# Performance work log

Hardware: AMD Instinct MI355X
Metric: run time of the kernel (lower is better)

## Reference

```python
import jax, jax.numpy as jnp
import numpy as np

B, T, D = 2, 2048, 1024
H = 16
DK = D // H


def setup_inputs() -> dict:
    key = jax.random.key(0)
    ks = jax.random.split(key, 5)
    s = 1.0 / np.sqrt(D)
    return {
        "x": jax.random.normal(ks[0], (B, T, D), dtype=jnp.float32),
        "Wq": jax.random.normal(ks[1], (D, D), dtype=jnp.float32) * s,
        "bq": jnp.zeros((D,), dtype=jnp.float32),
        "Wk": jax.random.normal(ks[2], (D, D), dtype=jnp.float32) * s,
        "bk": jnp.zeros((D,), dtype=jnp.float32),
        "Wv": jax.random.normal(ks[3], (D, D), dtype=jnp.float32) * s,
        "bv": jnp.zeros((D,), dtype=jnp.float32),
        "Wo": jax.random.normal(ks[4], (D, D), dtype=jnp.float32) * s,
        "bo": jnp.zeros((D,), dtype=jnp.float32),
    }


def reference(x, Wq, bq, Wk, bk, Wv, bv, Wo, bo):
    # projections (torch Linear: x @ W.T + b; here W is stored as (in, out))
    Q = x @ Wq + bq  # (B,T,D)
    K = x @ Wk + bk
    V = x @ Wv + bv
    # split heads -> (B,H,T,dk)
    Q = Q.reshape(B, T, H, DK).transpose(0, 2, 1, 3)
    K = K.reshape(B, T, H, DK).transpose(0, 2, 1, 3)
    V = V.reshape(B, T, H, DK).transpose(0, 2, 1, 3)
    scale = 1.0 / jnp.sqrt(jnp.asarray(DK, dtype=x.dtype))
    scores = jnp.einsum("bhqd,bhkd->bhqk", Q, K) * scale  # (B,H,T,T)
    causal = jnp.tril(jnp.ones((T, T), dtype=bool))
    scores = jnp.where(causal, scores, -jnp.inf)
    weights = jax.nn.softmax(scores, axis=-1)
    # dropout is identity in eval mode
    context = jnp.einsum("bhqk,bhkd->bhqd", weights, V)
    context = context.transpose(0, 2, 1, 3).reshape(B, T, D)
    return context @ Wo + bo
```

## Files before the change

kernel.cpp:

```cpp
#include <hip/hip_runtime.h>
#include <hip/hip_bf16.h>

constexpr int Bc = 2;
constexpr int Tc = 2048;
constexpr int Mc = Bc * Tc;
constexpr float CfQ = 0.18033688011112042f;

typedef __attribute__((ext_vector_type(8))) __bf16 bf16x8;
typedef __attribute__((ext_vector_type(4))) __bf16 bf16x4;
typedef __attribute__((ext_vector_type(4))) float floatx4;

__device__ __forceinline__ void gl_lds16(const void* g, void* l) {
    __builtin_amdgcn_global_load_lds(
        (const __attribute__((address_space(1))) void*)g,
        (__attribute__((address_space(3))) void*)l, 16, 0, 0);
}

__global__ __launch_bounds__(256) void prep_all(const float* __restrict__ x,
                                                const float* __restrict__ Wq,
                                                const float* __restrict__ Wk,
                                                const float* __restrict__ Wv,
                                                const float* __restrict__ Wo,
                                                __bf16* __restrict__ xb,
                                                __bf16* __restrict__ Wqkv,
                                                __bf16* __restrict__ Wot) {
    const int z = blockIdx.z;
    const int tid = threadIdx.x;
    if (z >= 4) {
        const int lb = blockIdx.y * 16 + blockIdx.x;
        const size_t base = ((size_t)(z - 4) * 256 + lb) * 4096;
#pragma unroll
        for (int it = 0; it < 4; ++it) {
            const size_t i = base + (size_t)(it * 256 + tid) * 4;
            const float4 v = *(const float4*)(x + i);
            bf16x4 r;
            r[0] = (__bf16)v.x; r[1] = (__bf16)v.y;
            r[2] = (__bf16)v.z; r[3] = (__bf16)v.w;
            *(bf16x4*)(xb + i) = r;
        }
        return;
    }
    __shared__ float t[64][65];
    const float* W = (z == 0) ? Wq : (z == 1) ? Wk : (z == 2) ? Wv : Wo;
    __bf16* Wt = (z < 3) ? Wqkv + (size_t)z * 1024 * 1024 : Wot;
    const int k0 = blockIdx.y * 64, n0 = blockIdx.x * 64;
    const int c = tid & 63, r0 = tid >> 6;
#pragma unroll
    for (int i = 0; i < 16; ++i)
        t[r0 + i * 4][c] = W[(size_t)(k0 + r0 + i * 4) * 1024 + n0 + c];
    __syncthreads();
#pragma unroll
    for (int i = 0; i < 16; ++i) {
        const int r = r0 + i * 4;
        Wt[(size_t)(n0 + r) * 1024 + k0 + c] = (__bf16)t[c][r];
    }
}

__global__ __launch_bounds__(256) void gemm_qkv(const __bf16* __restrict__ A,
                                                const __bf16* __restrict__ Bt,
                                                const float* __restrict__ b0,
                                                const float* __restrict__ b1,
                                                const float* __restrict__ b2,
                                                __bf16* __restrict__ C,
                                                __bf16* __restrict__ Vt) {
    constexpr int TN = 128, NI = 4, K = 1024, ldc = 2048;
    __shared__ __bf16 As[128 * 64];
    __shared__ __bf16 Bs[TN * 64];
    const int tid = threadIdx.x, lane = tid & 63, wave = tid >> 6;
    const int wm = wave & 1, wn = wave >> 1;
    const int bm = blockIdx.y * 128, bn = blockIdx.x * TN;
    const __bf16* Ab = A + (size_t)bm * K;
    const __bf16* Bb = Bt + (size_t)bn * K;
    const int quad = lane >> 4, tm = lane & 15;
    const int tsw = tm & 7;

    floatx4 acc[4][NI] = {};

    for (int k0 = 0; k0 < K; k0 += 64) {
#pragma unroll
        for (int i = 0; i < 4; ++i) {
            const int s = i * 256 + tid;
            const int row = s >> 3;
            const int lc = (s & 7) ^ (row & 7);
            gl_lds16(Ab + (size_t)row * K + k0 + lc * 8, As + s * 8);
        }
#pragma unroll
        for (int i = 0; i < 4; ++i) {
            const int s = i * 256 + tid;
            const int row = s >> 3;
            const int lc = (s & 7) ^ (row & 7);
            gl_lds16(Bb + (size_t)row * K + k0 + lc * 8, Bs + s * 8);
        }
        __syncthreads();
        bf16x8 af[4][2], bfv[NI][2];
#pragma unroll
        for (int mi = 0; mi < 4; ++mi) {
            const int row = (wm * 64 + mi * 16 + tm) * 64;
#pragma unroll
            for (int ks = 0; ks < 2; ++ks)
                af[mi][ks] = *(const bf16x8*)(As + row + ((ks * 4 + quad) ^ tsw) * 8);
        }
#pragma unroll
        for (int ni = 0; ni < NI; ++ni) {
            const int row = (wn * (TN / 2) + ni * 16 + tm) * 64;
#pragma unroll
            for (int ks = 0; ks < 2; ++ks)
                bfv[ni][ks] = *(const bf16x8*)(Bs + row + ((ks * 4 + quad) ^ tsw) * 8);
        }
#pragma unroll
        for (int ks = 0; ks < 2; ++ks)
#pragma unroll
            for (int mi = 0; mi < 4; ++mi)
#pragma unroll
                for (int ni = 0; ni < NI; ++ni)
                    acc[mi][ni] = __builtin_amdgcn_mfma_f32_16x16x32_bf16(
                        af[mi][ks], bfv[ni][ks], acc[mi][ni], 0, 0, 0);
        __syncthreads();
    }

#pragma unroll
    for (int ni = 0; ni < NI; ++ni) {
        const int gc = bn + wn * (TN / 2) + ni * 16 + tm;
        const float bias = (gc < 1024) ? b0[gc]
                         : (gc < 2048) ? b1[gc - 1024]
                                       : b2[gc - 2048];
        const float scale = (gc < 1024) ? CfQ : 1.0f;
#pragma unroll
        for (int mi = 0; mi < 4; ++mi) {
            const int gr0 = bm + wm * 64 + mi * 16 + quad * 4;
            if (gc >= 2048) {
                bf16x4 pv;
#pragma unroll
                for (int r = 0; r < 4; ++r) pv[r] = (__bf16)(acc[mi][ni][r] + bias);
                const int bb = gr0 >> 11, tloc = gr0 & 2047;
                const int hh = (gc - 2048) >> 6, dd = gc & 63;
                const int tperm = (tloc & ~63) + ((tloc >> 2) & 3) * 16 +
                                  ((tloc >> 4) & 3) * 4;
                *(bf16x4*)(Vt + ((size_t)(bb * 16 + hh) * 64 + dd) * 2048 + tperm) = pv;
            } else {
#pragma unroll
                for (int r = 0; r < 4; ++r)
                    C[(size_t)(gr0 + r) * ldc + gc] =
                        (__bf16)((acc[mi][ni][r] + bias) * scale);
            }
        }
    }
}

__global__ __launch_bounds__(256) void gemm_out(const __bf16* __restrict__ A,
                                                const __bf16* __restrict__ Bt,
                                                const float* __restrict__ b0,
                                                float* __restrict__ C) {
    constexpr int TN = 64, NI = 2, K = 1024, ldc = 1024;
    __shared__ __bf16 As[2][128 * 32];
    __shared__ __bf16 Bs[2][TN * 32];
    const int tid = threadIdx.x, lane = tid & 63, wave = tid >> 6;
    const int wm = wave & 1, wn = wave >> 1;
    const int bm = blockIdx.y * 128, bn = blockIdx.x * TN;
    const __bf16* Ab = A + (size_t)bm * K;
    const __bf16* Bb = Bt + (size_t)bn * K;
    const int quad = lane >> 4, tm = lane & 15;
    const int xsw = (tm >> 1) & 3;

    floatx4 acc[4][NI] = {};

    auto stage = [&](int k0, int sbuf) {
#pragma unroll
        for (int i = 0; i < 2; ++i) {
            const int s = i * 256 + tid;
            const int row = s >> 2;
            const int lc = (s & 3) ^ ((row >> 1) & 3);
            gl_lds16(Ab + (size_t)row * K + k0 + lc * 8, &As[sbuf][s * 8]);
        }
        {
            const int s = tid;
            const int row = s >> 2;
            const int lc = (s & 3) ^ ((row >> 1) & 3);
            gl_lds16(Bb + (size_t)row * K + k0 + lc * 8, &Bs[sbuf][s * 8]);
        }
    };

    const int nstep = K >> 5;
    stage(0, 0);
    stage(32, 1);

    for (int ks = 0; ks < nstep; ++ks) {
        const int buf = ks & 1;
        if (ks + 1 < nstep) {
            asm volatile("s_waitcnt vmcnt(3)" ::: "memory");
        } else {
            asm volatile("s_waitcnt vmcnt(0)" ::: "memory");
        }
        __builtin_amdgcn_sched_barrier(0);
        __builtin_amdgcn_s_barrier();

        bf16x8 af[4], bfv[NI];
#pragma unroll
        for (int mi = 0; mi < 4; ++mi)
            af[mi] = *(const bf16x8*)(&As[buf][(wm * 64 + mi * 16 + tm) * 32 +
                                               ((quad ^ xsw) * 8)]);
#pragma unroll
        for (int ni = 0; ni < NI; ++ni)
            bfv[ni] = *(const bf16x8*)(&Bs[buf][(wn * (TN / 2) + ni * 16 + tm) * 32 +
                                                ((quad ^ xsw) * 8)]);
        __builtin_amdgcn_s_setprio(1);
#pragma unroll
        for (int mi = 0; mi < 4; ++mi)
#pragma unroll
            for (int ni = 0; ni < NI; ++ni)
                acc[mi][ni] = __builtin_amdgcn_mfma_f32_16x16x32_bf16(
                    af[mi], bfv[ni], acc[mi][ni], 0, 0, 0);
        __builtin_amdgcn_s_setprio(0);
        __builtin_amdgcn_sched_barrier(0);
        __builtin_amdgcn_s_barrier();
        if (ks + 2 < nstep) stage((ks + 2) * 32, buf);
    }

#pragma unroll
    for (int ni = 0; ni < NI; ++ni) {
        const int gc = bn + wn * (TN / 2) + ni * 16 + tm;
        const float bias = b0[gc];
#pragma unroll
        for (int mi = 0; mi < 4; ++mi) {
            const int gr0 = bm + wm * 64 + mi * 16 + quad * 4;
#pragma unroll
            for (int r = 0; r < 4; ++r)
                C[(size_t)(gr0 + r) * ldc + gc] = acc[mi][ni][r] + bias;
        }
    }
}

__global__ __launch_bounds__(512, 4) void attn_mfma(const __bf16* __restrict__ QK,
                                                    const __bf16* __restrict__ Vt,
                                                    __bf16* __restrict__ ctx) {
    constexpr float NEG = -1e30f;

    __shared__ __bf16 Ks[2][2][64 * 64];
    __shared__ __bf16 Vts[2][2][64 * 64];

    const int tid = threadIdx.x, lane = tid & 63, w = tid >> 6;
    const int g = w >> 2, wq = w & 3;
    const int c = lane & 15, quad = lane >> 4;
    const int n = blockIdx.x;
    const int bh = (n & 7) * 4 + ((n >> 3) & 3);
    const int ip = n >> 5;
    const int b = bh >> 4, h = bh & 15;

    const __bf16* Qb = QK + (size_t)(b * Tc) * 2048 + h * 64;
    const __bf16* Kb = Qb + 1024;
    const __bf16* Vtb = Vt + (size_t)bh * 64 * 2048;

    const int sw = c & 7;
    int koff0[4], koff1[4];
#pragma unroll
    for (int ni = 0; ni < 4; ++ni) {
        const int krow = ni * 16 + c;
        koff0[ni] = krow * 64 + (quad ^ sw) * 8;
        koff1[ni] = krow * 64 + ((4 + quad) ^ sw) * 8;
    }
    int voff[4][2];
#pragma unroll
    for (int di = 0; di < 4; ++di) {
        const int vrow = di * 16 + c;
#pragma unroll
        for (int pr = 0; pr < 2; ++pr)
            voff[di][pr] = vrow * 64 + ((quad * 2 + pr) ^ sw) * 8;
    }

    const int srow = tid >> 3;
    const int slc = (tid & 7) ^ (srow & 7);
    const __bf16* kgB = Kb + (size_t)srow * 2048 + slc * 8;
    const __bf16* vgB = Vtb + (size_t)srow * 2048 + slc * 8;

#pragma unroll 1
    for (int ph = 0; ph < 2; ++ph) {
        const int qt = ph ? 31 - ip : ip;
        const int nk = qt + 1;
        const int npair = (nk + 1) >> 1;

        const __bf16* qr = Qb + (size_t)(qt * 64 + wq * 16 + c) * 2048;
        const bf16x8 qf0 = *(const bf16x8*)(qr + quad * 8);
        const bf16x8 qf1 = *(const bf16x8*)(qr + 32 + quad * 8);

        floatx4 lacc = {};
        floatx4 oa[4] = {};

        auto stage = [&](int p, int sbuf) {
            const __bf16* kg = kgB + (size_t)(2 * p) * 64 * 2048;
            const __bf16* vg = vgB + 2 * p * 64;
            __bf16* kd = &Ks[sbuf][0][tid * 8];
            __bf16* vd = &Vts[sbuf][0][tid * 8];
            gl_lds16(kg, kd);
            gl_lds16(kg + (size_t)64 * 2048, kd + 4096);
            gl_lds16(vg, vd);
            gl_lds16(vg + 64, vd + 4096);
        };

        stage(0, 0);
        if (npair > 1) stage(1, 1);

        for (int kp = 0; kp < npair; ++kp) {
            const int buf = kp & 1;
            if (kp + 1 < npair) {
                asm volatile("s_waitcnt vmcnt(4)" ::: "memory");
            } else {
                asm volatile("s_waitcnt vmcnt(0)" ::: "memory");
            }
            __builtin_amdgcn_sched_barrier(0);
            __builtin_amdgcn_s_barrier();

            const int kt = 2 * kp + g;
            if (kt < nk) {
                const __bf16* ks = Ks[buf][g];
                const __bf16* vs = Vts[buf][g];

                float sv[4][4];
                __builtin_amdgcn_s_setprio(1);
#pragma unroll
                for (int ni = 0; ni < 4; ++ni) {
                    const bf16x8 kb0 = *(const bf16x8*)(ks + koff0[ni]);
                    const bf16x8 kb1 = *(const bf16x8*)(ks + koff1[ni]);
                    floatx4 a = {};
                    a = __builtin_amdgcn_mfma_f32_16x16x32_bf16(kb0, qf0, a, 0, 0, 0);
                    a = __builtin_amdgcn_mfma_f32_16x16x32_bf16(kb1, qf1, a, 0, 0, 0);
#pragma unroll
                    for (int r = 0; r < 4; ++r) sv[ni][r] = a[r];
                }
                __builtin_amdgcn_s_setprio(0);

                if (kt == qt) {
#pragma unroll
                    for (int ni = 0; ni < 4; ++ni)
#pragma unroll
                        for (int r = 0; r < 4; ++r)
                            if (ni * 16 + quad * 4 + r > wq * 16 + c) sv[ni][r] = NEG;
                }
#pragma unroll
                for (int ni = 0; ni < 4; ++ni) {
#pragma unroll
                    for (int r = 0; r < 4; ++r) sv[ni][r] = __builtin_exp2f(sv[ni][r]);
                    lacc[0] += sv[ni][0];
                    lacc[1] += sv[ni][1];
                    lacc[2] += sv[ni][2];
                    lacc[3] += sv[ni][3];
                }

                bf16x8 pb[2];
#pragma unroll
                for (int pr = 0; pr < 2; ++pr)
#pragma unroll
                    for (int j = 0; j < 4; ++j) {
                        pb[pr][j] = (__bf16)sv[pr * 2][j];
                        pb[pr][4 + j] = (__bf16)sv[pr * 2 + 1][j];
                    }

                __builtin_amdgcn_s_setprio(1);
#pragma unroll
                for (int di = 0; di < 4; ++di) {
#pragma unroll
                    for (int pr = 0; pr < 2; ++pr) {
                        const bf16x8 vf = *(const bf16x8*)(vs + voff[di][pr]);
                        oa[di] = __builtin_amdgcn_mfma_f32_16x16x32_bf16(
                            vf, pb[pr], oa[di], 0, 0, 0);
                    }
                }
                __builtin_amdgcn_s_setprio(0);
            }
            __builtin_amdgcn_sched_barrier(0);
            __builtin_amdgcn_s_barrier();
            if (kp + 2 < npair) stage(kp + 2, buf);
        }

        __syncthreads();
        float lsum = lacc[0] + lacc[1] + lacc[2] + lacc[3];
        float* sc = (float*)&Ks[0][0][0];
        if (g == 1) {
#pragma unroll
            for (int di = 0; di < 4; ++di)
                *(floatx4*)(sc + wq * 1088 + di * 256 + lane * 4) = oa[di];
            sc[wq * 1088 + 1024 + lane] = lsum;
        }
        __syncthreads();
        if (g == 0) {
#pragma unroll
            for (int di = 0; di < 4; ++di)
                oa[di] += *(const floatx4*)(sc + wq * 1088 + di * 256 + lane * 4);
            lsum += sc[wq * 1088 + 1024 + lane];
            lsum += __shfl_xor(lsum, 16);
            lsum += __shfl_xor(lsum, 32);
            const float inv = 1.f / lsum;
            __bf16* cp = ctx + (size_t)(b * Tc + qt * 64 + wq * 16 + c) * 1024 +
                         h * 64 + quad * 4;
#pragma unroll
            for (int di = 0; di < 4; ++di) {
                bf16x4 rv;
#pragma unroll
                for (int r = 0; r < 4; ++r) rv[r] = (__bf16)(oa[di][r] * inv);
                *(bf16x4*)(cp + di * 16) = rv;
            }
        }
        __syncthreads();
    }
}

extern "C" void kernel_launch(void* const* d_in, const int* in_sizes, int n_in,
                              void* d_out, int out_size, void* d_ws, size_t ws_size,
                              hipStream_t stream) {
    const float* x  = (const float*)d_in[0];
    const float* Wq = (const float*)d_in[1];
    const float* bq = (const float*)d_in[2];
    const float* Wk = (const float*)d_in[3];
    const float* bk = (const float*)d_in[4];
    const float* Wv = (const float*)d_in[5];
    const float* bv = (const float*)d_in[6];
    const float* Wo = (const float*)d_in[7];
    const float* bo = (const float*)d_in[8];

    __bf16* xb   = (__bf16*)d_ws;
    __bf16* Wqkv = xb + (size_t)Mc * 1024;
    __bf16* Wot  = Wqkv + (size_t)3072 * 1024;
    __bf16* QKb  = Wot + (size_t)1024 * 1024;
    __bf16* Vtw  = QKb + (size_t)Mc * 2048;
    __bf16* ctxb = xb;

    prep_all<<<dim3(16, 16, 8), 256, 0, stream>>>(x, Wq, Wk, Wv, Wo,
                                                  xb, Wqkv, Wot);

    gemm_qkv<<<dim3(24, 32), 256, 0, stream>>>(xb, Wqkv, bq, bk, bv, QKb, Vtw);

    attn_mfma<<<dim3(512), 512, 0, stream>>>(QKb, Vtw, ctxb);

    gemm_out<<<dim3(16, 32), 256, 0, stream>>>(ctxb, Wot, bo, (float*)d_out);
}
```

Baseline: 190.7 us.

## Rework QKV GEMM into 256x256 tiles with double-buffered LDS pipeline

The QKV projection GEMM now uses 256x256 output tiles with 512 threads (8 waves, 2x4 layout) and a 1D grid of 192 blocks. The block index is remapped so that neighbouring blocks share A rows in cache. Global-to-LDS loads are double-buffered and the next K slice is prefetched while the current one is computed, using explicit vmcnt waits, s_barrier and setprio around the MFMA bursts. The aim is to hide load latency and raise arithmetic intensity per block. In exchange it uses 128KB of LDS per block and many more accumulator registers, and 192 blocks may underfill the 256 CUs.

New measurement: 189.8 us. Within noise of the previous version (-0.5%).

```diff
diff --git a/kernel.cpp b/kernel.cpp
--- a/kernel.cpp
+++ b/kernel.cpp
@@ -56,78 +56,111 @@
     }
 }
 
-__global__ __launch_bounds__(256) void gemm_qkv(const __bf16* __restrict__ A,
-                                                const __bf16* __restrict__ Bt,
-                                                const float* __restrict__ b0,
-                                                const float* __restrict__ b1,
-                                                const float* __restrict__ b2,
-                                                __bf16* __restrict__ C,
-                                                __bf16* __restrict__ Vt) {
-    constexpr int TN = 128, NI = 4, K = 1024, ldc = 2048;
-    __shared__ __bf16 As[128 * 64];
-    __shared__ __bf16 Bs[TN * 64];
+__global__ __launch_bounds__(512, 2) void gemm_qkv(const __bf16* __restrict__ A,
+                                                   const __bf16* __restrict__ Bt,
+                                                   const float* __restrict__ b0,
+                                                   const float* __restrict__ b1,
+                                                   const float* __restrict__ b2,
+                                                   __bf16* __restrict__ C,
+                                                   __bf16* __restrict__ Vt) {
+    constexpr int K = 1024, ldc = 2048;
+    __shared__ __bf16 As[2][256 * 64];
+    __shared__ __bf16 Bs[2][256 * 64];
     const int tid = threadIdx.x, lane = tid & 63, wave = tid >> 6;
-    const int wm = wave & 1, wn = wave >> 1;
-    const int bm = blockIdx.y * 128, bn = blockIdx.x * TN;
+    const int wm = wave >> 2, wn = wave & 3;
+    const int n = blockIdx.x;
+    const int xc = n & 7, ii = n >> 3;
+    const int by = 2 * xc + (ii & 1), bx = ii >> 1;
+    const int bm = by * 256, bn = bx * 256;
     const __bf16* Ab = A + (size_t)bm * K;
     const __bf16* Bb = Bt + (size_t)bn * K;
     const int quad = lane >> 4, tm = lane & 15;
-    const int tsw = tm & 7;
-
-    floatx4 acc[4][NI] = {};
-
-    for (int k0 = 0; k0 < K; k0 += 64) {
-#pragma unroll
-        for (int i = 0; i < 4; ++i) {
-            const int s = i * 256 + tid;
-            const int row = s >> 3;
-            const int lc = (s & 7) ^ (row & 7);
-            gl_lds16(Ab + (size_t)row * K + k0 + lc * 8, As + s * 8);
-        }
-#pragma unroll
-        for (int i = 0; i < 4; ++i) {
-            const int s = i * 256 + tid;
-            const int row = s >> 3;
-            const int lc = (s & 7) ^ (row & 7);
-            gl_lds16(Bb + (size_t)row * K + k0 + lc * 8, Bs + s * 8);
-        }
-        __syncthreads();
-        bf16x8 af[4][2], bfv[NI][2];
-#pragma unroll
-        for (int mi = 0; mi < 4; ++mi) {
-            const int row = (wm * 64 + mi * 16 + tm) * 64;
+
+    floatx4 acc[8][4] = {};
+
+    auto stage = [&](int k0, int sb) {
+#pragma unroll
+        for (int j = 0; j < 4; ++j) {
+            const int s = j * 512 + tid;
+            const int row = s >> 3, lc = (s & 7) ^ (row & 7);
+            gl_lds16(Ab + (size_t)row * K + k0 + lc * 8, &As[sb][s * 8]);
+        }
+#pragma unroll
+        for (int j = 0; j < 4; ++j) {
+            const int s = j * 512 + tid;
+            const int row = s >> 3, lc = (s & 7) ^ (row & 7);
+            gl_lds16(Bb + (size_t)row * K + k0 + lc * 8, &Bs[sb][s * 8]);
+        }
+    };
+
+    stage(0, 0);
+
+    bf16x8 afq[4][2];
+    for (int st = 0; st < 16; ++st) {
+        const int buf = st & 1;
+        if (st + 1 < 16) {
+            stage((st + 1) * 64, buf ^ 1);
+            asm volatile("s_waitcnt vmcnt(8)" ::: "memory");
+        } else {
+            asm volatile("s_waitcnt vmcnt(0)" ::: "memory");
+        }
+        __builtin_amdgcn_sched_barrier(0);
+        __builtin_amdgcn_s_barrier();
+
+        const __bf16* as = As[buf];
+        const __bf16* bs = Bs[buf];
+#pragma unroll
+        for (int p = 0; p < 4; ++p) {
+            const int qm = p >> 1, qn = p & 1;
+            if (qn == 0) {
+#pragma unroll
+                for (int m2 = 0; m2 < 4; ++m2) {
+                    const int r = wm * 128 + (qm * 4 + m2) * 16 + tm;
+#pragma unroll
+                    for (int ks = 0; ks < 2; ++ks)
+                        afq[m2][ks] = *(const bf16x8*)(
+                            as + r * 64 + (((ks * 4 + quad) ^ (r & 7)) * 8));
+                }
+            }
+            bf16x8 bfp[2][2];
+#pragma unroll
+            for (int n2 = 0; n2 < 2; ++n2) {
+                const int r = wn * 64 + (qn * 2 + n2) * 16 + tm;
+#pragma unroll
+                for (int ks = 0; ks < 2; ++ks)
+                    bfp[n2][ks] = *(const bf16x8*)(
+                        bs + r * 64 + (((ks * 4 + quad) ^ (r & 7)) * 8));
+            }
+            __builtin_amdgcn_s_barrier();
+            asm volatile("s_waitcnt lgkmcnt(0)" ::: "memory");
+            __builtin_amdgcn_sched_barrier(0);
+            __builtin_amdgcn_s_setprio(1);
 #pragma unroll
             for (int ks = 0; ks < 2; ++ks)
-                af[mi][ks] = *(const bf16x8*)(As + row + ((ks * 4 + quad) ^ tsw) * 8);
-        }
-#pragma unroll
-        for (int ni = 0; ni < NI; ++ni) {
-            const int row = (wn * (TN / 2) + ni * 16 + tm) * 64;
-#pragma unroll
-            for (int ks = 0; ks < 2; ++ks)
-                bfv[ni][ks] = *(const bf16x8*)(Bs + row + ((ks * 4 + quad) ^ tsw) * 8);
-        }
-#pragma unroll
-        for (int ks = 0; ks < 2; ++ks)
-#pragma unroll
-            for (int mi = 0; mi < 4; ++mi)
-#pragma unroll
-                for (int ni = 0; ni < NI; ++ni)
-                    acc[mi][ni] = __builtin_amdgcn_mfma_f32_16x16x32_bf16(
-                        af[mi][ks], bfv[ni][ks], acc[mi][ni], 0, 0, 0);
-        __syncthreads();
-    }
-
-#pragma unroll
-    for (int ni = 0; ni < NI; ++ni) {
-        const int gc = bn + wn * (TN / 2) + ni * 16 + tm;
+#pragma unroll
+                for (int m2 = 0; m2 < 4; ++m2)
+#pragma unroll
+                    for (int n2 = 0; n2 < 2; ++n2)
+                        acc[qm * 4 + m2][qn * 2 + n2] =
+                            __builtin_amdgcn_mfma_f32_16x16x32_bf16(
+                                afq[m2][ks], bfp[n2][ks],
+                                acc[qm * 4 + m2][qn * 2 + n2], 0, 0, 0);
+            __builtin_amdgcn_s_setprio(0);
+            __builtin_amdgcn_sched_barrier(0);
+        }
+        __builtin_amdgcn_s_barrier();
+    }
+
+#pragma unroll
+    for (int ni = 0; ni < 4; ++ni) {
+        const int gc = bn + wn * 64 + ni * 16 + tm;
         const float bias = (gc < 1024) ? b0[gc]
                          : (gc < 2048) ? b1[gc - 1024]
                                        : b2[gc - 2048];
         const float scale = (gc < 1024) ? CfQ : 1.0f;
 #pragma unroll
-        for (int mi = 0; mi < 4; ++mi) {
-            const int gr0 = bm + wm * 64 + mi * 16 + quad * 4;
+        for (int mi = 0; mi < 8; ++mi) {
+            const int gr0 = bm + wm * 128 + mi * 16 + quad * 4;
             if (gc >= 2048) {
                 bf16x4 pv;
 #pragma unroll
@@ -426,7 +459,7 @@
     prep_all<<<dim3(16, 16, 8), 256, 0, stream>>>(x, Wq, Wk, Wv, Wo,
                                                   xb, Wqkv, Wot);
 
-    gemm_qkv<<<dim3(24, 32), 256, 0, stream>>>(xb, Wqkv, bq, bk, bv, QKb, Vtw);
+    gemm_qkv<<<dim3(192), 512, 0, stream>>>(xb, Wqkv, bq, bk, bv, QKb, Vtw);
 
     attn_mfma<<<dim3(512), 512, 0, stream>>>(QKb, Vtw, ctxb);
 
```
